# Kernel optimization log

Measured on AMD Instinct MI355X. Metric: run time of the kernel, lower is better.

Reference implementation:

```python
import jax, jax.numpy as jnp
import numpy as np

SCALE_BASE = 512
EPS = 1e-5


def _xpos_factors(seq_len, head_dim):
    half = head_dim // 2
    # xpos scale vector: ((arange(0, hd, 2) + 0.4*hd) / (1.4*hd)) ** (pos / scale_base)
    s = (jnp.arange(0, head_dim, 2, dtype=jnp.float32) + 0.4 * head_dim) / (1.4 * head_dim)
    pos = jnp.arange(seq_len, dtype=jnp.float32)
    scale = s[None, :] ** (pos[:, None] / SCALE_BASE)          # (S, half)
    inv_freq = 1.0 / (10000.0 ** (jnp.arange(half, dtype=jnp.float32) / half))
    ang = pos[:, None] * inv_freq[None, :]                     # (S, half)
    return jnp.sin(ang), jnp.cos(ang), scale


def _dup_interleave(m):
    # (S, half) -> (S, head_dim): each column duplicated, interleaved
    return jnp.repeat(m, 2, axis=-1)


def _rotate_every_two(x):
    x1, x2 = x[..., ::2], x[..., 1::2]
    return jnp.stack((-x2, x1), axis=-1).reshape(x.shape)


def _apply_xpos(x, sin, cos, scale):
    sinf = _dup_interleave(sin * scale)                        # (S, hd)
    cosf = _dup_interleave(cos * scale)
    return x * cosf + _rotate_every_two(x) * sinf


def _decay_mask(gammas, seq_len, chunk_size):
    # D[h, i, j] = gamma_h ** |i - j| if j < ((i // chunk) + 1) * chunk else 0
    i = jnp.arange(seq_len)[:, None]
    j = jnp.arange(seq_len)[None, :]
    allowed = j < ((i // chunk_size) + 1) * chunk_size         # (S, S)
    expo = jnp.abs(i - j).astype(jnp.float32)
    D = gammas[:, None, None] ** expo[None]                    # (H, S, S)
    return jnp.where(allowed[None], D, 0.0)


def setup_inputs() -> dict:
    key = jax.random.key(0)
    B, S, hidden, H, hd, chunk = 4, 2048, 512, 8, 64, 64
    ks = jax.random.split(key, 6)
    return {
        "X": jax.random.normal(ks[0], (B, S, hidden), dtype=jnp.float32),
        "W_Q": jax.random.normal(ks[1], (H, hidden, hd), dtype=jnp.float32) / hidden,
        "W_K": jax.random.normal(ks[2], (H, hidden, hd), dtype=jnp.float32) / hidden,
        "W_V": jax.random.normal(ks[3], (H, hidden, hd), dtype=jnp.float32) / hidden,
        "W_G": jax.random.normal(ks[4], (hidden, H * hd), dtype=jnp.float32) / hidden,
        "W_O": jax.random.normal(ks[5], (H * hd, hidden), dtype=jnp.float32) / hidden,
        "gn_weight": jnp.ones((H * hd,), dtype=jnp.float32),
        "gn_bias": jnp.zeros((H * hd,), dtype=jnp.float32),
        "chunk_size": chunk,
    }


def reference(X, W_Q, W_K, W_V, W_G, W_O, gn_weight, gn_bias, chunk_size):
    B, S, hidden = X.shape
    H, _, hd = W_Q.shape
    # RetNet multi-scale decay rates
    gammas = 1.0 - jnp.exp(
        jnp.linspace(jnp.log(jnp.float32(1 / 32)), jnp.log(jnp.float32(1 / 512)), H)
    )
    D = _decay_mask(gammas, S, chunk_size)                     # (H, S, S)

    # per-head projections: n = heads
    Q = jnp.einsum("bsh,nhd->bnsd", X, W_Q)
    K = jnp.einsum("bsh,nhd->bnsd", X, W_K)
    V = jnp.einsum("bsh,nhd->bnsd", X, W_V)

    sin, cos, scale = _xpos_factors(S, hd)
    Q = _apply_xpos(Q, sin, cos, scale)                        # broadcast (S,hd) over (B,H,S,hd)
    K = _apply_xpos(K, sin, cos, 1.0 / scale)                  # downscale

    scores = jnp.einsum("bnsd,bntd->bnst", Q, K) * D[None]     # (B,H,S,S)
    Yh = jnp.einsum("bnst,bntd->bnsd", scores, V)              # (B,H,S,hd)

    # concat heads -> (B,S,H*hd), GroupNorm(heads) per token (stats over each head's hd channels)
    Y = Yh.transpose(0, 2, 1, 3)                               # (B,S,H,hd)
    mu = Y.mean(-1, keepdims=True)
    var = Y.var(-1, keepdims=True)
    Yn = (Y - mu) / jnp.sqrt(var + EPS)
    Yn = Yn.reshape(B, S, H * hd) * gn_weight + gn_bias

    gate = jax.nn.silu(X @ W_G)                                # swish(X W_G)
    return (gate * Yn) @ W_O
```

## Files before the change

kernel.cpp:

```cpp
#include <hip/hip_runtime.h>

#define B_   4
#define S_   2048
#define HID  512
#define H_   8
#define HD   64

typedef __attribute__((ext_vector_type(8))) short bf16x8;
typedef __attribute__((ext_vector_type(4))) float f32x4;

#define MFMA16(a, b, c) __builtin_amdgcn_mfma_f32_16x16x32_bf16(a, b, c, 0, 0, 0)

#define GAMMA_L0   (-3.4657359027997265f)
#define GAMMA_STEP (-0.3960841031771116f)

__device__ __forceinline__ void async16(const void* g, void* l) {
    __builtin_amdgcn_global_load_lds(
        (const __attribute__((address_space(1))) void*)g,
        (__attribute__((address_space(3))) void*)l, 16, 0, 0);
}

__device__ __forceinline__ unsigned short f2bf(float x) {
    unsigned u = __float_as_uint(x);
    return (unsigned short)((u + 0x7fffu + ((u >> 16) & 1u)) >> 16);
}
__device__ __forceinline__ float bfs2f(short s) {
    return __uint_as_float(((unsigned)(unsigned short)s) << 16);
}
__device__ __forceinline__ unsigned packbf(float lo, float hi) {
    return (unsigned)f2bf(lo) | ((unsigned)f2bf(hi) << 16);
}

__global__ __launch_bounds__(256) void prep(
    const float* __restrict__ X,
    const float* __restrict__ Wq, const float* __restrict__ Wk,
    const float* __restrict__ Wv, const float* __restrict__ Wg,
    const float* __restrict__ Wo,
    short* __restrict__ Xb,
    short* __restrict__ WqT, short* __restrict__ WkT, short* __restrict__ WvT,
    short* __restrict__ WgT, short* __restrict__ WoT,
    float4* __restrict__ Lut)
{
    __shared__ float T[64][65];
    const int bid = blockIdx.x, t = threadIdx.x;

    if (bid < 2048) {
        size_t i = ((size_t)bid * 256 + t) * 8;
        float4 a = *(const float4*)&X[i];
        float4 b = *(const float4*)&X[i + 4];
        union { int4 v; unsigned short s[8]; } u;
        u.s[0] = f2bf(a.x); u.s[1] = f2bf(a.y); u.s[2] = f2bf(a.z); u.s[3] = f2bf(a.w);
        u.s[4] = f2bf(b.x); u.s[5] = f2bf(b.y); u.s[6] = f2bf(b.z); u.s[7] = f2bf(b.w);
        *(int4*)&Xb[i] = u.v;
        return;
    }
    if (bid >= 2368) {
        int idx = (bid - 2368) * 256 + t;
        int s = idx >> 5, k = idx & 31;
        float invf = exp2f(-0.41524101186092035f * (float)k);
        float ang  = (float)s * invf;
        float sn = sinf(ang), cs = cosf(ang);
        float sk = ((float)(2 * k) + 25.6f) / 89.6f;
        float sc = exp2f(log2f(sk) * (float)s * (1.0f / 512.0f));
        Lut[idx] = (float4){cs * sc, sn * sc, cs / sc, sn / sc};
        return;
    }

    const int wb = bid - 2048;
    const float* ip; short* op; int ild;
    if (wb < 192) {
        int which = wb >> 6, rem = wb & 63, h = rem >> 3, kt = rem & 7;
        const float* src = which == 0 ? Wq : which == 1 ? Wk : Wv;
        short* dst       = which == 0 ? WqT : which == 1 ? WkT : WvT;
        ip = src + ((size_t)h * 512 + kt * 64) * 64;
        ild = 64;
        op = dst + (size_t)(h * 64) * 512 + kt * 64;
    } else {
        int rem = wb - 192, which = rem >> 6, r3 = rem & 63, nt = r3 >> 3, kt = r3 & 7;
        const float* src = which ? Wo : Wg;
        short* dst       = which ? WoT : WgT;
        ip = src + (size_t)(kt * 64) * 512 + nt * 64;
        ild = 512;
        op = dst + (size_t)(nt * 64) * 512 + kt * 64;
    }
    {
        int r = t >> 2, c0 = (t & 3) * 16;
        #pragma unroll
        for (int e = 0; e < 4; ++e) {
            float4 f = *(const float4*)&ip[(size_t)r * ild + c0 + e * 4];
            T[r][c0 + e*4 + 0] = f.x; T[r][c0 + e*4 + 1] = f.y;
            T[r][c0 + e*4 + 2] = f.z; T[r][c0 + e*4 + 3] = f.w;
        }
    }
    __syncthreads();
    {
        int cc = t >> 2, r0 = (t & 3) * 16;
        short* orow = op + (size_t)cc * 512;
        #pragma unroll
        for (int ii = 0; ii < 8; ++ii) {
            int lo = f2bf(T[r0 + 2*ii][cc]);
            int hi = f2bf(T[r0 + 2*ii + 1][cc]);
            *(int*)(orow + r0 + 2*ii) = (lo & 0xffff) | (hi << 16);
        }
    }
}

__device__ __forceinline__ void stage64k(const short* __restrict__ Ag,
                                         const short* __restrict__ Bg,
                                         int k0, short* As, short* Bs, int tid)
{
    #pragma unroll
    for (int j = 0; j < 2; ++j) {
        int idx = j * 256 + tid;
        int row = idx >> 3, c8 = (idx & 7) ^ (row & 7);
        async16(Ag + (size_t)row * 512 + k0 + c8 * 8, As + idx * 8);
    }
    #pragma unroll
    for (int j = 0; j < 4; ++j) {
        int idx = j * 256 + tid;
        int row = idx >> 3, c8 = (idx & 7) ^ (row & 7);
        async16(Bg + (size_t)row * 512 + k0 + c8 * 8, Bs + idx * 8);
    }
}

__device__ __forceinline__ void gemm_core64(const short* __restrict__ Ag,
                                            const short* __restrict__ Bg,
                                            short* SM, f32x4 (&acc)[2][4])
{
    const int tid = threadIdx.x;
    const int L = tid & 63, quad = L >> 4, l16 = L & 15;
    const int w = tid >> 6;
    const int wrow = (w >> 1) * 32, wcol = (w & 1) * 64;
    short* As = SM;
    short* Bs = SM + 4096;

    for (int k0 = 0; k0 < 512; k0 += 64) {
        stage64k(Ag, Bg, k0, As, Bs, tid);
        __syncthreads();
        #pragma unroll
        for (int ks = 0; ks < 2; ++ks) {
            bf16x8 af[2], bfr[4];
            #pragma unroll
            for (int a = 0; a < 2; ++a) {
                int m = wrow + a * 16 + l16;
                af[a] = *(const bf16x8*)&As[m * 64 + ((quad + 4 * ks) ^ (m & 7)) * 8];
            }
            #pragma unroll
            for (int b = 0; b < 4; ++b) {
                int n = wcol + b * 16 + l16;
                bfr[b] = *(const bf16x8*)&Bs[n * 64 + ((quad + 4 * ks) ^ (n & 7)) * 8];
            }
            #pragma unroll
            for (int a = 0; a < 2; ++a)
                #pragma unroll
                for (int b = 0; b < 4; ++b)
                    acc[a][b] = MFMA16(af[a], bfr[b], acc[a][b]);
        }
        __syncthreads();
    }
}

__global__ __launch_bounds__(256) void fused_gemm(
    const short* __restrict__ Xb, const short* __restrict__ WT,
    const float4* __restrict__ Lut,
    short* __restrict__ Qb, short* __restrict__ Kb, short* __restrict__ Vb,
    short* __restrict__ Gb)
{
    __shared__ short SM[12288];
    const int by = blockIdx.x;
    const int bx = blockIdx.y;

    f32x4 acc[2][4];
    #pragma unroll
    for (int a = 0; a < 2; ++a)
        #pragma unroll
        for (int b = 0; b < 4; ++b) acc[a][b] = (f32x4){0.f, 0.f, 0.f, 0.f};

    gemm_core64(Xb + (size_t)by * 64 * 512,
                WT + (size_t)bx * 128 * 512, SM, acc);

    const int tid = threadIdx.x, L = tid & 63, quad = L >> 4, l16 = L & 15;
    const int w = tid >> 6, wrow = (w >> 1) * 32, wcol = (w & 1) * 64;
    const int zone = bx >> 2;
    short* Out = (zone == 0) ? Qb : (zone == 1) ? Kb : Vb;

    #pragma unroll
    for (int b = 0; b < 4; ++b) {
        int ncol = (bx & 3) * 128 + wcol + b * 16 + l16;
        int d = ncol & 63, k = d >> 1;
        int colE = wcol + b * 16 + (l16 & ~1);
        #pragma unroll
        for (int a = 0; a < 2; ++a) {
            #pragma unroll
            for (int r = 0; r < 4; ++r) {
                int m = by * 64 + wrow + a * 16 + quad * 4 + r;
                int s = m & 2047;
                float v = acc[a][b][r];
                unsigned word;
                if (zone == 3) {
                    float g = v / (1.0f + __expf(-v));
                    float part = __shfl_xor(g, 1);
                    word = packbf(g, part);
                } else {
                    float part = __shfl_xor(v, 1);
                    float e = (d & 1) ? part : v;
                    float o = (d & 1) ? v : part;
                    if (zone == 2) {
                        word = packbf(e, o);
                    } else {
                        float4 f = Lut[s * 32 + k];
                        float cs = (zone == 0) ? f.x : f.z;
                        float sn = (zone == 0) ? f.y : f.w;
                        word = packbf(e * cs - o * sn, o * cs + e * sn);
                    }
                }
                if (!(l16 & 1))
                    *(int*)&SM[(wrow + a * 16 + quad * 4 + r) * 136 + colE] = word;
            }
        }
    }
    __syncthreads();
    #pragma unroll
    for (int j = 0; j < 4; ++j) {
        int idx = j * 256 + tid;
        int row = idx >> 4, c0 = (idx & 15) * 8;
        int m = by * 64 + row;
        int n = (bx & 3) * 128 + c0;
        if (zone == 3) {
            *(int4*)&Gb[(size_t)m * 512 + n] = *(const int4*)&SM[row * 136 + c0];
        } else {
            int bb = m >> 11, s = m & 2047;
            int h = n >> 6, d = n & 63;
            *(int4*)&Out[(((size_t)bb * 8 + h) * 2048 + s) * 64 + d] =
                *(const int4*)&SM[row * 136 + c0];
        }
    }
}

__global__ __launch_bounds__(256) void out_gemm(
    const short* __restrict__ Zb, const short* __restrict__ WoT,
    float* __restrict__ Of)
{
    __shared__ short SM[8192];
    const int by = blockIdx.x;
    const int bx = blockIdx.y;

    f32x4 acc[2][2];
    #pragma unroll
    for (int a = 0; a < 2; ++a)
        #pragma unroll
        for (int b = 0; b < 2; ++b) acc[a][b] = (f32x4){0.f, 0.f, 0.f, 0.f};

    const int tid = threadIdx.x;
    const int L = tid & 63, quad = L >> 4, l16 = L & 15;
    const int w = tid >> 6;
    const int wrow = (w >> 1) * 32, wcol = (w & 1) * 32;
    const short* Ag = Zb + (size_t)by * 64 * 512;
    const short* Bg = WoT + (size_t)bx * 64 * 512;
    short* As = SM;
    short* Bs = SM + 4096;

    for (int k0 = 0; k0 < 512; k0 += 64) {
        #pragma unroll
        for (int j = 0; j < 2; ++j) {
            int idx = j * 256 + tid;
            int row = idx >> 3, c8 = (idx & 7) ^ (row & 7);
            async16(Ag + (size_t)row * 512 + k0 + c8 * 8, As + idx * 8);
            async16(Bg + (size_t)row * 512 + k0 + c8 * 8, Bs + idx * 8);
        }
        __syncthreads();
        #pragma unroll
        for (int ks = 0; ks < 2; ++ks) {
            bf16x8 af[2], bfr[2];
            #pragma unroll
            for (int a = 0; a < 2; ++a) {
                int m = wrow + a * 16 + l16;
                af[a] = *(const bf16x8*)&As[m * 64 + ((quad + 4 * ks) ^ (m & 7)) * 8];
            }
            #pragma unroll
            for (int b = 0; b < 2; ++b) {
                int n = wcol + b * 16 + l16;
                bfr[b] = *(const bf16x8*)&Bs[n * 64 + ((quad + 4 * ks) ^ (n & 7)) * 8];
            }
            #pragma unroll
            for (int a = 0; a < 2; ++a)
                #pragma unroll
                for (int b = 0; b < 2; ++b)
                    acc[a][b] = MFMA16(af[a], bfr[b], acc[a][b]);
        }
        __syncthreads();
    }

    #pragma unroll
    for (int b = 0; b < 2; ++b) {
        int ncol = bx * 64 + wcol + b * 16 + l16;
        #pragma unroll
        for (int a = 0; a < 2; ++a)
            #pragma unroll
            for (int r = 0; r < 4; ++r) {
                int m = by * 64 + wrow + a * 16 + quad * 4 + r;
                Of[(size_t)m * 512 + ncol] = acc[a][b][r];
            }
    }
}

__global__ __launch_bounds__(256) void ret_g(
    const short* __restrict__ Kb, const short* __restrict__ Vb,
    short* __restrict__ Gt)
{
    __shared__ short Kt[64 * 72];
    __shared__ short Vt[64 * 72];
    const int tid = threadIdx.x, L = tid & 63, quad = L >> 4, l16 = L & 15;
    const int w = tid >> 6;
    const int c = blockIdx.x, bn = blockIdx.y, hh = bn & 7;

    float gamma = 1.0f - expf(GAMMA_L0 + GAMMA_STEP * (float)hh);
    float lg = log2f(gamma);

    {
        const short* kg = Kb + ((size_t)bn * 2048 + c * 64 + L) * 64 + w * 16;
        const short* vg = Vb + ((size_t)bn * 2048 + c * 64 + L) * 64 + w * 16;
        float wgt = exp2f(lg * (float)(64 - L));
        int4 k0 = *(const int4*)kg; int4 k1 = *(const int4*)(kg + 8);
        int4 v0 = *(const int4*)vg; int4 v1 = *(const int4*)(vg + 8);
        short* kt = Kt + L; short* vt = Vt + L;
        #pragma unroll
        for (int q = 0; q < 4; ++q) {
            int uk = ((const int*)&k0)[q];
            kt[(w*16 + 2*q)     * 72] = (short)f2bf(bfs2f((short)uk) * wgt);
            kt[(w*16 + 2*q + 1) * 72] = (short)f2bf(bfs2f((short)(uk >> 16)) * wgt);
            int uv = ((const int*)&v0)[q];
            vt[(w*16 + 2*q)     * 72] = (short)uv;
            vt[(w*16 + 2*q + 1) * 72] = (short)(uv >> 16);
        }
        #pragma unroll
        for (int q = 0; q < 4; ++q) {
            int uk = ((const int*)&k1)[q];
            kt[(w*16 + 8 + 2*q) * 72] = (short)f2bf(bfs2f((short)uk) * wgt);
            kt[(w*16 + 9 + 2*q) * 72] = (short)f2bf(bfs2f((short)(uk >> 16)) * wgt);
            int uv = ((const int*)&v1)[q];
            vt[(w*16 + 8 + 2*q) * 72] = (short)uv;
            vt[(w*16 + 9 + 2*q) * 72] = (short)(uv >> 16);
        }
    }
    __syncthreads();

    bf16x8 a0 = *(const bf16x8*)&Vt[(w * 16 + l16) * 72 + quad * 8];
    bf16x8 a1 = *(const bf16x8*)&Vt[(w * 16 + l16) * 72 + 32 + quad * 8];
    short* Gp = Gt + ((size_t)bn * 32 + c) * 4096;
    #pragma unroll
    for (int b = 0; b < 4; ++b) {
        bf16x8 b0 = *(const bf16x8*)&Kt[(b * 16 + l16) * 72 + quad * 8];
        bf16x8 b1 = *(const bf16x8*)&Kt[(b * 16 + l16) * 72 + 32 + quad * 8];
        f32x4 acc = (f32x4){0.f, 0.f, 0.f, 0.f};
        acc = MFMA16(a0, b0, acc);
        acc = MFMA16(a1, b1, acc);
        #pragma unroll
        for (int r = 0; r < 4; ++r) {
            float v = acc[r];
            float part = __shfl_xor(v, 1);
            unsigned word = packbf(v, part);
            if (!(l16 & 1))
                *(int*)&Gp[(w*16 + quad*4 + r) * 64 + b * 16 + (l16 & ~1)] = word;
        }
    }
}

__global__ __launch_bounds__(256) void ret_scan(short* __restrict__ GM)
{
    const int tid = threadIdx.x, seg = blockIdx.x, bn = blockIdx.y, hh = bn & 7;
    float gamma = 1.0f - expf(GAMMA_L0 + GAMMA_STEP * (float)hh);
    float g64 = exp2f(log2f(gamma) * 64.0f);

    size_t base = (size_t)bn * 32 * 4096 + seg * 1024 + tid * 4;
    float m0 = 0.f, m1 = 0.f, m2 = 0.f, m3 = 0.f;
    #pragma unroll 4
    for (int c = 0; c < 32; ++c) {
        int2* p = (int2*)&GM[base + (size_t)c * 4096];
        int2 g = *p;
        *p = make_int2((int)packbf(m0, m1), (int)packbf(m2, m3));
        m0 = g64 * m0 + bfs2f((short)g.x);
        m1 = g64 * m1 + bfs2f((short)(g.x >> 16));
        m2 = g64 * m2 + bfs2f((short)g.y);
        m3 = g64 * m3 + bfs2f((short)(g.y >> 16));
    }
}

__global__ __launch_bounds__(256) void ret_main(
    const short* __restrict__ Qb, const short* __restrict__ Kb,
    const short* __restrict__ Vb, const short* __restrict__ Mb,
    const short* __restrict__ Gb,
    const float* __restrict__ gw, const float* __restrict__ gb,
    short* __restrict__ Zb)
{
    __shared__ short Qs[4096];
    __shared__ short Ks[4096];
    __shared__ short Ms[4096];
    __shared__ short Vt[64 * 72];
    __shared__ short Pw[4][16 * 72];

    const int tid = threadIdx.x, L = tid & 63, quad = L >> 4, l16 = L & 15;
    const int w = tid >> 6;
    const int c = blockIdx.x, bn = blockIdx.y, hh = bn & 7, bb = bn >> 3;

    float gamma = 1.0f - expf(GAMMA_L0 + GAMMA_STEP * (float)hh);
    float lg = log2f(gamma);

    float Dabs[4][4];
    #pragma unroll
    for (int b = 0; b < 4; ++b)
        #pragma unroll
        for (int r = 0; r < 4; ++r) {
            int dlt = (w * 16 + quad * 4 + r) - (b * 16 + l16);
            Dabs[b][r] = exp2f(lg * fabsf((float)dlt));
        }
    float gq[4];
    #pragma unroll
    for (int r = 0; r < 4; ++r)
        gq[r] = exp2f(lg * (float)(w * 16 + quad * 4 + r));

    {
        const short* qg = Qb + ((size_t)bn * 2048 + c * 64 + w * 16 + (L >> 2)) * 64 + (L & 3) * 8;
        async16(qg,      Qs + w * 512 + L * 8);
        async16(qg + 32, Qs + 2048 + w * 512 + L * 8);
        const short* kg = Kb + ((size_t)bn * 2048 + c * 64 + w * 16 + (L >> 2)) * 64 + (L & 3) * 8;
        async16(kg,      Ks + w * 512 + L * 8);
        async16(kg + 32, Ks + 2048 + w * 512 + L * 8);
        const short* mg = Mb + ((size_t)bn * 32 + c) * 4096 + (w * 16 + (L >> 2)) * 64 + (L & 3) * 8;
        async16(mg,      Ms + w * 512 + L * 8);
        async16(mg + 32, Ms + 2048 + w * 512 + L * 8);
    }
    {
        const short* vg = Vb + ((size_t)bn * 2048 + c * 64 + L) * 64 + w * 16;
        int4 v0 = *(const int4*)vg;
        int4 v1 = *(const int4*)(vg + 8);
        short* vt = Vt + L;
        #pragma unroll
        for (int q = 0; q < 4; ++q) {
            int u = ((const int*)&v0)[q];
            vt[(w*16 + 2*q)     * 72] = (short)u;
            vt[(w*16 + 2*q + 1) * 72] = (short)(u >> 16);
        }
        #pragma unroll
        for (int q = 0; q < 4; ++q) {
            int u = ((const int*)&v1)[q];
            vt[(w*16 + 8 + 2*q) * 72] = (short)u;
            vt[(w*16 + 9 + 2*q) * 72] = (short)(u >> 16);
        }
    }
    __syncthreads();

    bf16x8 aQ0 = *(const bf16x8*)&Qs[(w * 16 + l16) * 32 + quad * 8];
    bf16x8 aQ1 = *(const bf16x8*)&Qs[2048 + (w * 16 + l16) * 32 + quad * 8];
    f32x4 accM[4];
    #pragma unroll
    for (int b = 0; b < 4; ++b) {
        bf16x8 k0 = *(const bf16x8*)&Ks[(b * 16 + l16) * 32 + quad * 8];
        bf16x8 k1 = *(const bf16x8*)&Ks[2048 + (b * 16 + l16) * 32 + quad * 8];
        f32x4 S = (f32x4){0.f, 0.f, 0.f, 0.f};
        S = MFMA16(aQ0, k0, S);
        S = MFMA16(aQ1, k1, S);
        #pragma unroll
        for (int r = 0; r < 4; ++r)
            Pw[w][(quad * 4 + r) * 72 + b * 16 + l16] = (short)f2bf(S[r] * Dabs[b][r]);

        bf16x8 m0 = *(const bf16x8*)&Ms[(b * 16 + l16) * 32 + quad * 8];
        bf16x8 m1 = *(const bf16x8*)&Ms[2048 + (b * 16 + l16) * 32 + quad * 8];
        f32x4 Mv = (f32x4){0.f, 0.f, 0.f, 0.f};
        Mv = MFMA16(aQ0, m0, Mv);
        Mv = MFMA16(aQ1, m1, Mv);
        accM[b] = Mv;
    }

    bf16x8 aP0 = *(const bf16x8*)&Pw[w][l16 * 72 + quad * 8];
    bf16x8 aP1 = *(const bf16x8*)&Pw[w][l16 * 72 + 32 + quad * 8];
    f32x4 Y4[4];
    #pragma unroll
    for (int b2 = 0; b2 < 4; ++b2) {
        bf16x8 v0f = *(const bf16x8*)&Vt[(b2 * 16 + l16) * 72 + quad * 8];
        bf16x8 v1f = *(const bf16x8*)&Vt[(b2 * 16 + l16) * 72 + 32 + quad * 8];
        f32x4 yv = (f32x4){0.f, 0.f, 0.f, 0.f};
        yv = MFMA16(aP0, v0f, yv);
        yv = MFMA16(aP1, v1f, yv);
        #pragma unroll
        for (int r = 0; r < 4; ++r)
            Y4[b2][r] = yv[r] + gq[r] * accM[b2][r];
    }

    #pragma unroll
    for (int r = 0; r < 4; ++r) {
        float s1 = 0.f, s2 = 0.f;
        #pragma unroll
        for (int b2 = 0; b2 < 4; ++b2) {
            float v = Y4[b2][r];
            s1 += v; s2 += v * v;
        }
        #pragma unroll
        for (int off = 1; off < 16; off <<= 1) {
            s1 += __shfl_xor(s1, off);
            s2 += __shfl_xor(s2, off);
        }
        float mu = s1 * (1.0f / 64.0f);
        float var = s2 * (1.0f / 64.0f) - mu * mu;
        float rstd = rsqrtf(var + 1e-5f);

        int il = w * 16 + quad * 4 + r;
        size_t row = (size_t)bb * 2048 + c * 64 + il;
        #pragma unroll
        for (int b2 = 0; b2 < 4; ++b2) {
            int j = hh * 64 + b2 * 16 + l16;
            float yn = (Y4[b2][r] - mu) * rstd * gw[j] + gb[j];
            float z = bfs2f(Gb[row * 512 + j]) * yn;
            float part = __shfl_xor(z, 1);
            if (!(l16 & 1))
                *(int*)&Zb[row * 512 + hh * 64 + b2 * 16 + (l16 & ~1)] = packbf(z, part);
        }
    }
}

extern "C" void kernel_launch(void* const* d_in, const int* in_sizes, int n_in,
                              void* d_out, int out_size, void* d_ws, size_t ws_size,
                              hipStream_t stream)
{
    const float* X  = (const float*)d_in[0];
    const float* Wq = (const float*)d_in[1];
    const float* Wk = (const float*)d_in[2];
    const float* Wv = (const float*)d_in[3];
    const float* Wg = (const float*)d_in[4];
    const float* Wo = (const float*)d_in[5];
    const float* gw = (const float*)d_in[6];
    const float* gb = (const float*)d_in[7];

    char* ws = (char*)d_ws;
    short* Xb  = (short*)ws;
    short* WqT = (short*)(ws + 8388608);
    short* WkT = WqT + 262144;
    short* WvT = WkT + 262144;
    short* WgT = WvT + 262144;
    short* WoT = WgT + 262144;
    short* Qb  = (short*)(ws + 11010048);
    short* Kb  = Qb + 4194304;
    short* Vb  = Kb + 4194304;
    float4* Lut = (float4*)(ws + 36175872);
    short* GM  = (short*)(ws + 37224448);
    short* Zb  = (short*)(ws + 45613056);
    short* Gb  = (short*)(ws + 54001664);

    prep<<<2624, 256, 0, stream>>>(X, Wq, Wk, Wv, Wg, Wo,
                                   Xb, WqT, WkT, WvT, WgT, WoT, Lut);
    fused_gemm<<<dim3(128, 16), 256, 0, stream>>>(Xb, WqT, Lut, Qb, Kb, Vb, Gb);
    ret_g<<<dim3(32, 32), 256, 0, stream>>>(Kb, Vb, GM);
    ret_scan<<<dim3(4, 32), 256, 0, stream>>>(GM);
    ret_main<<<dim3(32, 32), 256, 0, stream>>>(Qb, Kb, Vb, GM, Gb, gw, gb, Zb);
    out_gemm<<<dim3(128, 8), 256, 0, stream>>>(Zb, WoT, (float*)d_out);
}
```

Baseline: 162.8 us.

## Store V transposed from projection GEMM and async-load it in retention kernels

```diff
diff --git a/kernel.cpp b/kernel.cpp
--- a/kernel.cpp
+++ b/kernel.cpp
@@ -182,7 +182,6 @@
     const int tid = threadIdx.x, L = tid & 63, quad = L >> 4, l16 = L & 15;
     const int w = tid >> 6, wrow = (w >> 1) * 32, wcol = (w & 1) * 64;
     const int zone = bx >> 2;
-    short* Out = (zone == 0) ? Qb : (zone == 1) ? Kb : Vb;
 
     #pragma unroll
     for (int b = 0; b < 4; ++b) {
@@ -220,19 +219,38 @@
         }
     }
     __syncthreads();
-    #pragma unroll
-    for (int j = 0; j < 4; ++j) {
-        int idx = j * 256 + tid;
-        int row = idx >> 4, c0 = (idx & 15) * 8;
-        int m = by * 64 + row;
-        int n = (bx & 3) * 128 + c0;
-        if (zone == 3) {
-            *(int4*)&Gb[(size_t)m * 512 + n] = *(const int4*)&SM[row * 136 + c0];
-        } else {
-            int bb = m >> 11, s = m & 2047;
+
+    if (zone == 2) {
+        #pragma unroll
+        for (int j = 0; j < 4; ++j) {
+            int idx = j * 256 + tid;
+            int col = idx >> 3, sg = idx & 7;
+            int n = (bx & 3) * 128 + col;
             int h = n >> 6, d = n & 63;
-            *(int4*)&Out[(((size_t)bb * 8 + h) * 2048 + s) * 64 + d] =
-                *(const int4*)&SM[row * 136 + c0];
+            int m0 = by * 64 + sg * 8;
+            int bb = m0 >> 11, s0 = m0 & 2047;
+            union { int4 v; short s[8]; } u;
+            #pragma unroll
+            for (int e = 0; e < 8; ++e)
+                u.s[e] = SM[(sg * 8 + e) * 136 + col];
+            *(int4*)&Vb[(((size_t)bb * 8 + h) * 64 + d) * 2048 + s0] = u.v;
+        }
+    } else {
+        short* Out = (zone == 0) ? Qb : Kb;
+        #pragma unroll
+        for (int j = 0; j < 4; ++j) {
+            int idx = j * 256 + tid;
+            int row = idx >> 4, c0 = (idx & 15) * 8;
+            int m = by * 64 + row;
+            int n = (bx & 3) * 128 + c0;
+            if (zone == 3) {
+                *(int4*)&Gb[(size_t)m * 512 + n] = *(const int4*)&SM[row * 136 + c0];
+            } else {
+                int bb = m >> 11, s = m & 2047;
+                int h = n >> 6, d = n & 63;
+                *(int4*)&Out[(((size_t)bb * 8 + h) * 2048 + s) * 64 + d] =
+                    *(const int4*)&SM[row * 136 + c0];
+            }
         }
     }
 }
@@ -309,7 +327,7 @@
     short* __restrict__ Gt)
 {
     __shared__ short Kt[64 * 72];
-    __shared__ short Vt[64 * 72];
+    __shared__ short Vs[4096];
     const int tid = threadIdx.x, L = tid & 63, quad = L >> 4, l16 = L & 15;
     const int w = tid >> 6;
     const int c = blockIdx.x, bn = blockIdx.y, hh = bn & 7;
@@ -318,35 +336,32 @@
     float lg = log2f(gamma);
 
     {
+        const short* vg = Vb + ((size_t)bn * 64 + w * 16 + (L >> 2)) * 2048 + c * 64 + (L & 3) * 8;
+        async16(vg,      Vs + w * 512 + L * 8);
+        async16(vg + 32, Vs + 2048 + w * 512 + L * 8);
+    }
+    {
         const short* kg = Kb + ((size_t)bn * 2048 + c * 64 + L) * 64 + w * 16;
-        const short* vg = Vb + ((size_t)bn * 2048 + c * 64 + L) * 64 + w * 16;
         float wgt = exp2f(lg * (float)(64 - L));
         int4 k0 = *(const int4*)kg; int4 k1 = *(const int4*)(kg + 8);
-        int4 v0 = *(const int4*)vg; int4 v1 = *(const int4*)(vg + 8);
-        short* kt = Kt + L; short* vt = Vt + L;
+        short* kt = Kt + L;
         #pragma unroll
         for (int q = 0; q < 4; ++q) {
             int uk = ((const int*)&k0)[q];
             kt[(w*16 + 2*q)     * 72] = (short)f2bf(bfs2f((short)uk) * wgt);
             kt[(w*16 + 2*q + 1) * 72] = (short)f2bf(bfs2f((short)(uk >> 16)) * wgt);
-            int uv = ((const int*)&v0)[q];
-            vt[(w*16 + 2*q)     * 72] = (short)uv;
-            vt[(w*16 + 2*q + 1) * 72] = (short)(uv >> 16);
         }
         #pragma unroll
         for (int q = 0; q < 4; ++q) {
             int uk = ((const int*)&k1)[q];
             kt[(w*16 + 8 + 2*q) * 72] = (short)f2bf(bfs2f((short)uk) * wgt);
             kt[(w*16 + 9 + 2*q) * 72] = (short)f2bf(bfs2f((short)(uk >> 16)) * wgt);
-            int uv = ((const int*)&v1)[q];
-            vt[(w*16 + 8 + 2*q) * 72] = (short)uv;
-            vt[(w*16 + 9 + 2*q) * 72] = (short)(uv >> 16);
         }
     }
     __syncthreads();
 
-    bf16x8 a0 = *(const bf16x8*)&Vt[(w * 16 + l16) * 72 + quad * 8];
-    bf16x8 a1 = *(const bf16x8*)&Vt[(w * 16 + l16) * 72 + 32 + quad * 8];
+    bf16x8 a0 = *(const bf16x8*)&Vs[(w * 16 + l16) * 32 + quad * 8];
+    bf16x8 a1 = *(const bf16x8*)&Vs[2048 + (w * 16 + l16) * 32 + quad * 8];
     short* Gp = Gt + ((size_t)bn * 32 + c) * 4096;
     #pragma unroll
     for (int b = 0; b < 4; ++b) {
@@ -372,17 +387,15 @@
     float gamma = 1.0f - expf(GAMMA_L0 + GAMMA_STEP * (float)hh);
     float g64 = exp2f(log2f(gamma) * 64.0f);
 
-    size_t base = (size_t)bn * 32 * 4096 + seg * 1024 + tid * 4;
-    float m0 = 0.f, m1 = 0.f, m2 = 0.f, m3 = 0.f;
-    #pragma unroll 4
+    size_t base = (size_t)bn * 32 * 4096 + ((size_t)seg * 256 + tid) * 2;
+    float m0 = 0.f, m1 = 0.f;
+    #pragma unroll 8
     for (int c = 0; c < 32; ++c) {
-        int2* p = (int2*)&GM[base + (size_t)c * 4096];
-        int2 g = *p;
-        *p = make_int2((int)packbf(m0, m1), (int)packbf(m2, m3));
-        m0 = g64 * m0 + bfs2f((short)g.x);
-        m1 = g64 * m1 + bfs2f((short)(g.x >> 16));
-        m2 = g64 * m2 + bfs2f((short)g.y);
-        m3 = g64 * m3 + bfs2f((short)(g.y >> 16));
+        int* p = (int*)&GM[base + (size_t)c * 4096];
+        int g = *p;
+        *p = (int)packbf(m0, m1);
+        m0 = g64 * m0 + bfs2f((short)g);
+        m1 = g64 * m1 + bfs2f((short)(g >> 16));
     }
 }
 
@@ -396,7 +409,7 @@
     __shared__ short Qs[4096];
     __shared__ short Ks[4096];
     __shared__ short Ms[4096];
-    __shared__ short Vt[64 * 72];
+    __shared__ short Vs[4096];
     __shared__ short Pw[4][16 * 72];
 
     const int tid = threadIdx.x, L = tid & 63, quad = L >> 4, l16 = L & 15;
@@ -429,24 +442,9 @@
         const short* mg = Mb + ((size_t)bn * 32 + c) * 4096 + (w * 16 + (L >> 2)) * 64 + (L & 3) * 8;
         async16(mg,      Ms + w * 512 + L * 8);
         async16(mg + 32, Ms + 2048 + w * 512 + L * 8);
-    }
-    {
-        const short* vg = Vb + ((size_t)bn * 2048 + c * 64 + L) * 64 + w * 16;
-        int4 v0 = *(const int4*)vg;
-        int4 v1 = *(const int4*)(vg + 8);
-        short* vt = Vt + L;
-        #pragma unroll
-        for (int q = 0; q < 4; ++q) {
-            int u = ((const int*)&v0)[q];
-            vt[(w*16 + 2*q)     * 72] = (short)u;
-            vt[(w*16 + 2*q + 1) * 72] = (short)(u >> 16);
-        }
-        #pragma unroll
-        for (int q = 0; q < 4; ++q) {
-            int u = ((const int*)&v1)[q];
-            vt[(w*16 + 8 + 2*q) * 72] = (short)u;
-            vt[(w*16 + 9 + 2*q) * 72] = (short)(u >> 16);
-        }
+        const short* vg = Vb + ((size_t)bn * 64 + w * 16 + (L >> 2)) * 2048 + c * 64 + (L & 3) * 8;
+        async16(vg,      Vs + w * 512 + L * 8);
+        async16(vg + 32, Vs + 2048 + w * 512 + L * 8);
     }
     __syncthreads();
 
@@ -477,8 +475,8 @@
     f32x4 Y4[4];
     #pragma unroll
     for (int b2 = 0; b2 < 4; ++b2) {
-        bf16x8 v0f = *(const bf16x8*)&Vt[(b2 * 16 + l16) * 72 + quad * 8];
-        bf16x8 v1f = *(const bf16x8*)&Vt[(b2 * 16 + l16) * 72 + 32 + quad * 8];
+        bf16x8 v0f = *(const bf16x8*)&Vs[(b2 * 16 + l16) * 32 + quad * 8];
+        bf16x8 v1f = *(const bf16x8*)&Vs[2048 + (b2 * 16 + l16) * 32 + quad * 8];
         f32x4 yv = (f32x4){0.f, 0.f, 0.f, 0.f};
         yv = MFMA16(aP0, v0f, yv);
         yv = MFMA16(aP1, v1f, yv);
@@ -550,7 +548,7 @@
                                    Xb, WqT, WkT, WvT, WgT, WoT, Lut);
     fused_gemm<<<dim3(128, 16), 256, 0, stream>>>(Xb, WqT, Lut, Qb, Kb, Vb, Gb);
     ret_g<<<dim3(32, 32), 256, 0, stream>>>(Kb, Vb, GM);
-    ret_scan<<<dim3(4, 32), 256, 0, stream>>>(GM);
+    ret_scan<<<dim3(8, 32), 256, 0, stream>>>(GM);
     ret_main<<<dim3(32, 32), 256, 0, stream>>>(Qb, Kb, Vb, GM, Gb, gw, gb, Zb);
     out_gemm<<<dim3(128, 8), 256, 0, stream>>>(Zb, WoT, (float*)d_out);
 }
```

Measured after the change: 163.5 us. No clear change (+0.4%).
